# Kernel tuning notes

Measured on AMD Instinct MI355X. Metric: run time of the kernel, lower is better.

The kernel has to match this reference:

```python
import jax, jax.numpy as jnp
import numpy as np

D_MODEL = 1024
NHEAD = 16
D_K = D_MODEL // NHEAD


def setup_inputs() -> dict:
    key = jax.random.key(0)
    ks = jax.random.split(key, 12)
    B, S = 4, 2048
    s = 1.0 / np.sqrt(D_MODEL)
    inp = {
        'query': jax.random.normal(ks[0], (B, S, D_MODEL), jnp.float32),
        'key': jax.random.normal(ks[1], (B, S, D_MODEL), jnp.float32),
        'value': jax.random.normal(ks[2], (B, S, D_MODEL), jnp.float32),
        'Wq': jax.random.uniform(ks[3], (D_MODEL, D_MODEL), jnp.float32, -s, s),
        'bq': jax.random.uniform(ks[4], (D_MODEL,), jnp.float32, -s, s),
        'Wk': jax.random.uniform(ks[5], (D_MODEL, D_MODEL), jnp.float32, -s, s),
        'bk': jax.random.uniform(ks[6], (D_MODEL,), jnp.float32, -s, s),
        'Wv': jax.random.uniform(ks[7], (D_MODEL, D_MODEL), jnp.float32, -s, s),
        'bv': jax.random.uniform(ks[8], (D_MODEL,), jnp.float32, -s, s),
        'Wo': jax.random.uniform(ks[9], (D_MODEL, D_MODEL), jnp.float32, -s, s),
        'bo': jax.random.uniform(ks[10], (D_MODEL,), jnp.float32, -s, s),
    }
    return inp


def _split_heads(x, B):
    # (B, S, d_model) -> (B, H, S, d_k)
    return x.reshape(B, -1, NHEAD, D_K).transpose(0, 2, 1, 3)


def reference(query, key, value, Wq, bq, Wk, bk, Wv, bv, Wo, bo):
    B = query.shape[0]
    scale = np.sqrt(D_K).astype(np.float32)
    # torch Linear: y = x @ W.T + b
    Q = _split_heads(query @ Wq.T + bq, B)   # (B, H, Sq, d_k)
    K = _split_heads(key @ Wk.T + bk, B)     # (B, H, Sk, d_k)
    V = _split_heads(value @ Wv.T + bv, B)   # (B, H, Sk, d_k)
    scores = jnp.einsum('bhqd,bhkd->bhqk', Q, K) / scale
    attn = jax.nn.softmax(scores, axis=-1)   # dropout p=0 -> identity
    out = jnp.einsum('bhqk,bhkd->bhqd', attn, V)
    out = out.transpose(0, 2, 1, 3).reshape(B, -1, D_MODEL)
    return out @ Wo.T + bo
```

## Files before the change

kernel.cpp:

```cpp
#include <hip/hip_runtime.h>
#include <stdint.h>

typedef __attribute__((ext_vector_type(8))) _Float16 half8;
typedef __attribute__((ext_vector_type(2))) __fp16   fp16x2;
typedef __attribute__((ext_vector_type(4))) float    f32x4;
typedef __attribute__((ext_vector_type(4))) unsigned short us4;

__device__ __forceinline__ unsigned short f2h(float f) {
  union { _Float16 h; unsigned short u; } cv; cv.h = (_Float16)f; return cv.u;
}

__device__ __forceinline__ void async_copy16(void* lds, const void* g) {
  __builtin_amdgcn_global_load_lds(
      (__attribute__((address_space(1))) void*)(void*)g,
      (__attribute__((address_space(3))) void*)lds, 16, 0, 0);
}

union U64 { fp16x2 h2[2]; us4 u4; };

__global__ __launch_bounds__(256) void cvt_all(
    const float* __restrict__ q, const float* __restrict__ k, const float* __restrict__ v,
    const float* __restrict__ wq, const float* __restrict__ wk,
    const float* __restrict__ wv, const float* __restrict__ wo,
    unsigned short* __restrict__ oq, unsigned short* __restrict__ ok,
    unsigned short* __restrict__ ov,
    unsigned short* __restrict__ owq, unsigned short* __restrict__ owk,
    unsigned short* __restrict__ owv, unsigned short* __restrict__ owo) {
  int b = blockIdx.x;
  const float* in; unsigned short* out;
  if      (b < 8192)  { in = q;  out = oq;             }
  else if (b < 16384) { in = k;  out = ok;  b -= 8192; }
  else if (b < 24576) { in = v;  out = ov;  b -= 16384; }
  else if (b < 25600) { in = wq; out = owq; b -= 24576; }
  else if (b < 26624) { in = wk; out = owk; b -= 25600; }
  else if (b < 27648) { in = wv; out = owv; b -= 26624; }
  else                { in = wo; out = owo; b -= 27648; }
  const int i = (b * 256 + threadIdx.x) * 4;
  const float4 x = *(const float4*)(in + i);
  us4 o; o.x = f2h(x.x); o.y = f2h(x.y); o.z = f2h(x.z); o.w = f2h(x.w);
  *(us4*)(out + i) = o;
}

__device__ __forceinline__ void gemm128_core(const unsigned short* __restrict__ A,
                                             const unsigned short* __restrict__ Bw,
                                             int m0, int n0,
                                             unsigned short* As, unsigned short* Bs,
                                             f32x4 acc[4][4]) {
  const int tid  = threadIdx.x;
  const int w    = tid >> 6;
  const int l15  = tid & 15;
  const int quad = (tid >> 4) & 3;
  const int w0 = w & 1, w1 = w >> 1;
  const f32x4 zero4 = {0.f, 0.f, 0.f, 0.f};
#pragma unroll
  for (int mt = 0; mt < 4; ++mt)
#pragma unroll
    for (int nt = 0; nt < 4; ++nt) acc[mt][nt] = zero4;

  int srcR[2], srcC[2];
#pragma unroll
  for (int c = 0; c < 2; ++c) {
    const int idx = c * 256 + tid;
    srcR[c] = idx >> 2;
    srcC[c] = (idx & 3) ^ (srcR[c] & 3) ^ ((srcR[c] >> 2) & 3);
  }
  const int cs = quad ^ (l15 & 3) ^ (l15 >> 2);

  for (int k0 = 0; k0 < 1024; k0 += 32) {
    __syncthreads();
#pragma unroll
    for (int c = 0; c < 2; ++c) {
      async_copy16((char*)As + c * 4096 + w * 1024,
                   A  + (m0 + srcR[c]) * 1024 + k0 + srcC[c] * 8);
      async_copy16((char*)Bs + c * 4096 + w * 1024,
                   Bw + (n0 + srcR[c]) * 1024 + k0 + srcC[c] * 8);
    }
    __syncthreads();
    half8 af[4], bf[4];
#pragma unroll
    for (int mt = 0; mt < 4; ++mt)
      af[mt] = *(const half8*)(As + (w1 * 64 + mt * 16 + l15) * 32 + cs * 8);
#pragma unroll
    for (int nt = 0; nt < 4; ++nt)
      bf[nt] = *(const half8*)(Bs + (w0 * 64 + nt * 16 + l15) * 32 + cs * 8);
#pragma unroll
    for (int mt = 0; mt < 4; ++mt)
#pragma unroll
      for (int nt = 0; nt < 4; ++nt)
        acc[mt][nt] = __builtin_amdgcn_mfma_f32_16x16x32_f16(af[mt], bf[nt], acc[mt][nt], 0, 0, 0);
  }
}

__global__ __launch_bounds__(256) void gemm_qkv(
    const unsigned short* __restrict__ Xq, const unsigned short* __restrict__ Xk,
    const unsigned short* __restrict__ Xv,
    const unsigned short* __restrict__ Wq, const unsigned short* __restrict__ Wk,
    const unsigned short* __restrict__ Wv,
    const float* __restrict__ bq, const float* __restrict__ bk, const float* __restrict__ bv,
    unsigned short* __restrict__ Qo, unsigned short* __restrict__ Ko,
    unsigned short* __restrict__ Vo) {
  __shared__ __align__(16) unsigned short As[128 * 32];
  __shared__ __align__(16) unsigned short Bs[128 * 32];
  const int z = blockIdx.z;
  const unsigned short* A = (z == 0) ? Xq : (z == 1) ? Xk : Xv;
  const unsigned short* W = (z == 0) ? Wq : (z == 1) ? Wk : Wv;
  const float* bias = (z == 0) ? bq : (z == 1) ? bk : bv;
  const int m0 = blockIdx.x * 128, n0 = blockIdx.y * 128;
  f32x4 acc[4][4];
  gemm128_core(A, W, m0, n0, As, Bs, acc);

  const int tid = threadIdx.x;
  const int w = tid >> 6, l15 = tid & 15, quad = (tid >> 4) & 3;
  const int w0 = w & 1, w1 = w >> 1;
  const float qscale = (z == 0) ? 0.18033688011112042f : 1.0f;
#pragma unroll
  for (int mt = 0; mt < 4; ++mt) {
    const int mbase = m0 + w1 * 64 + mt * 16 + quad * 4;
    const int bb = mbase >> 11, s = mbase & 2047;
#pragma unroll
    for (int nt = 0; nt < 4; ++nt) {
      const int col = n0 + w0 * 64 + nt * 16 + l15;
      const float badd = bias[col];
      const int h = col >> 6, d = col & 63;
      if (z < 2) {
        unsigned short* dst = (z == 0) ? Qo : Ko;
#pragma unroll
        for (int r = 0; r < 4; ++r)
          dst[((bb * 16 + h) * 2048 + (s + r)) * 64 + d] = f2h((acc[mt][nt][r] + badd) * qscale);
      } else {
        us4 pk;
#pragma unroll
        for (int r = 0; r < 4; ++r) pk[r] = f2h(acc[mt][nt][r] + badd);
        *(us4*)(Vo + ((bb * 16 + h) * 64 + d) * 2048 + s) = pk;
      }
    }
  }
}

#define PKS 40
__global__ __launch_bounds__(512, 4) void attn_kernel(const unsigned short* __restrict__ Q,
                                                      const unsigned short* __restrict__ K,
                                                      const unsigned short* __restrict__ Vt,
                                                      unsigned short* __restrict__ O) {
  __shared__ __align__(16) unsigned short Ps[10240];
  __shared__ __align__(16) unsigned short Ks[2][64 * 64];
  __shared__ __align__(16) unsigned short Vs[2][64 * 64];
  const int bh = blockIdx.x, qt = blockIdx.y;
  const int tid = threadIdx.x;
  const int w = tid >> 6, l15 = tid & 15, quad = (tid >> 4) & 3;
  const int cq0 = quad ^ (l15 & 7), cq1 = (4 + quad) ^ (l15 & 7);

  const int srcR = tid >> 3;
  const int srcC = (tid & 7) ^ (srcR & 7);

  const unsigned short* Kg0 = K + bh * 2048 * 64;
  const unsigned short* Vg0 = Vt + bh * 131072;

  auto stage_kv = [&](int t, int buf) {
    async_copy16((char*)Ks + buf * 8192 + w * 1024, Kg0 + t * 4096 + srcR * 64 + srcC * 8);
    async_copy16((char*)Vs + buf * 8192 + w * 1024, Vg0 + t * 64 + srcR * 2048 + srcC * 8);
  };

  stage_kv(0, 0);
  const unsigned short* Qg = Q + (bh * 2048 + qt * 256) * 64;
  half8 qf[2][2];
#pragma unroll
  for (int s = 0; s < 2; ++s) {
    const int row = w * 32 + s * 16 + l15;
    qf[s][0] = *(const half8*)(Qg + row * 64 + quad * 8);
    qf[s][1] = *(const half8*)(Qg + row * 64 + 32 + quad * 8);
  }
  __syncthreads();

  const f32x4 zero4 = {0.f, 0.f, 0.f, 0.f};
  f32x4 acc[2][4];
  f32x4 lsum[2];
#pragma unroll
  for (int s = 0; s < 2; ++s) {
    lsum[s] = zero4;
#pragma unroll
    for (int dt = 0; dt < 4; ++dt) acc[s][dt] = zero4;
  }
  half8 ones;
#pragma unroll
  for (int i = 0; i < 8; ++i) ones[i] = (_Float16)1.0f;

  unsigned short* Pw = Ps + w * 1280;

  for (int kt = 0; kt < 32; ++kt) {
    if (kt < 31) stage_kv(kt + 1, (kt + 1) & 1);
    const unsigned short* Kc = Ks[kt & 1];
    const unsigned short* Vc = Vs[kt & 1];

#pragma unroll
    for (int h = 0; h < 2; ++h) {
#pragma unroll
      for (int nt2 = 0; nt2 < 2; ++nt2) {
        const int rk = (h * 2 + nt2) * 16 + l15;
        half8 ak0 = *(const half8*)(Kc + rk * 64 + cq0 * 8);
        half8 ak1 = *(const half8*)(Kc + rk * 64 + cq1 * 8);
#pragma unroll
        for (int s = 0; s < 2; ++s) {
          f32x4 z = zero4;
          z = __builtin_amdgcn_mfma_f32_16x16x32_f16(ak0, qf[s][0], z, 0, 0, 0);
          z = __builtin_amdgcn_mfma_f32_16x16x32_f16(ak1, qf[s][1], z, 0, 0, 0);
          U64 u;
          u.h2[0] = __builtin_amdgcn_cvt_pkrtz(__builtin_exp2f(z[0]), __builtin_exp2f(z[1]));
          u.h2[1] = __builtin_amdgcn_cvt_pkrtz(__builtin_exp2f(z[2]), __builtin_exp2f(z[3]));
          *(us4*)(Pw + s * 640 + l15 * PKS + nt2 * 16 + quad * 4) = u.u4;
        }
      }
      const int ch = h ? cq1 : cq0;
      half8 bp[2];
#pragma unroll
      for (int s = 0; s < 2; ++s) {
        bp[s] = *(const half8*)(Pw + s * 640 + l15 * PKS + quad * 8);
        lsum[s] = __builtin_amdgcn_mfma_f32_16x16x32_f16(ones, bp[s], lsum[s], 0, 0, 0);
      }
#pragma unroll
      for (int dt = 0; dt < 4; ++dt) {
        half8 av = *(const half8*)(Vc + (dt * 16 + l15) * 64 + ch * 8);
#pragma unroll
        for (int s = 0; s < 2; ++s)
          acc[s][dt] = __builtin_amdgcn_mfma_f32_16x16x32_f16(av, bp[s], acc[s][dt], 0, 0, 0);
      }
    }
    __syncthreads();
  }

  const int b = bh >> 4, hd = bh & 15;
#pragma unroll
  for (int s = 0; s < 2; ++s) {
    const float rv = 1.0f / lsum[s][0];
    const int sg = qt * 256 + w * 32 + s * 16 + l15;
    unsigned short* Orow = O + (b * 2048 + sg) * 1024 + hd * 64;
#pragma unroll
    for (int dt = 0; dt < 4; ++dt) {
      U64 u;
      u.h2[0] = __builtin_amdgcn_cvt_pkrtz(acc[s][dt][0] * rv, acc[s][dt][1] * rv);
      u.h2[1] = __builtin_amdgcn_cvt_pkrtz(acc[s][dt][2] * rv, acc[s][dt][3] * rv);
      *(us4*)(Orow + dt * 16 + quad * 4) = u.u4;
    }
  }
}

__global__ __launch_bounds__(256) void gemm_out(const unsigned short* __restrict__ A,
                                                const unsigned short* __restrict__ W,
                                                const float* __restrict__ bias,
                                                float* __restrict__ out) {
  __shared__ __align__(16) unsigned short As[128 * 32];
  __shared__ __align__(16) unsigned short Bs[128 * 32];
  const int m0 = blockIdx.x * 128, n0 = blockIdx.y * 128;
  f32x4 acc[4][4];
  gemm128_core(A, W, m0, n0, As, Bs, acc);
  const int tid = threadIdx.x;
  const int w = tid >> 6, l15 = tid & 15, quad = (tid >> 4) & 3;
  const int w0 = w & 1, w1 = w >> 1;
#pragma unroll
  for (int mt = 0; mt < 4; ++mt) {
    const int mbase = m0 + w1 * 64 + mt * 16 + quad * 4;
#pragma unroll
    for (int nt = 0; nt < 4; ++nt) {
      const int col = n0 + w0 * 64 + nt * 16 + l15;
      const float badd = bias[col];
#pragma unroll
      for (int r = 0; r < 4; ++r)
        out[(mbase + r) * 1024 + col] = acc[mt][nt][r] + badd;
    }
  }
}

extern "C" void kernel_launch(void* const* d_in, const int* in_sizes, int n_in,
                              void* d_out, int out_size, void* d_ws, size_t ws_size,
                              hipStream_t stream) {
  const float* query = (const float*)d_in[0];
  const float* key_  = (const float*)d_in[1];
  const float* value = (const float*)d_in[2];
  const float* Wq = (const float*)d_in[3];
  const float* bq = (const float*)d_in[4];
  const float* Wk = (const float*)d_in[5];
  const float* bk = (const float*)d_in[6];
  const float* Wv = (const float*)d_in[7];
  const float* bv = (const float*)d_in[8];
  const float* Wo = (const float*)d_in[9];
  const float* bo = (const float*)d_in[10];

  unsigned short* ws = (unsigned short*)d_ws;
  unsigned short* xq = ws;
  unsigned short* xk = xq + 8388608;
  unsigned short* xv = xk + 8388608;
  unsigned short* wq = xv + 8388608;
  unsigned short* wk = wq + 1048576;
  unsigned short* wv = wk + 1048576;
  unsigned short* wo = wv + 1048576;
  unsigned short* Qw = wo + 1048576;
  unsigned short* Kw = Qw + 8388608;
  unsigned short* Vw = Kw + 8388608;
  unsigned short* Ow = xq;

  cvt_all<<<28672, 256, 0, stream>>>(query, key_, value, Wq, Wk, Wv, Wo,
                                     xq, xk, xv, wq, wk, wv, wo);
  gemm_qkv<<<dim3(64, 8, 3), 256, 0, stream>>>(xq, xk, xv, wq, wk, wv, bq, bk, bv, Qw, Kw, Vw);
  attn_kernel<<<dim3(64, 8), 512, 0, stream>>>(Qw, Kw, Vw, Ow);
  gemm_out<<<dim3(64, 8), 256, 0, stream>>>(Ow, wo, bo, (float*)d_out);
}
```

Before: 357.0 us.

## Use 1024-thread attention blocks with one 16-row query tile per wave

The attention kernel moves from 8 waves each owning 32 query rows to 16 waves each owning 16 rows, so every wave holds half the accumulators and Q fragments. K/V staging is split so the first 512 threads load K and the rest load V. This cuts per-thread register pressure and adds more waves for latency hiding. The cost is that each loaded K/V fragment is reused across fewer query rows, so there is more LDS read traffic per FLOP, and a 1024-thread block synchronises more waves at each barrier.

```diff
diff --git a/kernel.cpp b/kernel.cpp
--- a/kernel.cpp
+++ b/kernel.cpp
@@ -138,10 +138,10 @@
 }
 
 #define PKS 40
-__global__ __launch_bounds__(512, 4) void attn_kernel(const unsigned short* __restrict__ Q,
-                                                      const unsigned short* __restrict__ K,
-                                                      const unsigned short* __restrict__ Vt,
-                                                      unsigned short* __restrict__ O) {
+__global__ __launch_bounds__(1024, 8) void attn_kernel(const unsigned short* __restrict__ Q,
+                                                       const unsigned short* __restrict__ K,
+                                                       const unsigned short* __restrict__ Vt,
+                                                       unsigned short* __restrict__ O) {
   __shared__ __align__(16) unsigned short Ps[10240];
   __shared__ __align__(16) unsigned short Ks[2][64 * 64];
   __shared__ __align__(16) unsigned short Vs[2][64 * 64];
@@ -150,42 +150,42 @@
   const int w = tid >> 6, l15 = tid & 15, quad = (tid >> 4) & 3;
   const int cq0 = quad ^ (l15 & 7), cq1 = (4 + quad) ^ (l15 & 7);
 
-  const int srcR = tid >> 3;
-  const int srcC = (tid & 7) ^ (srcR & 7);
+  const int t9 = tid & 511;
+  const int srcR = t9 >> 3;
+  const int srcC = (t9 & 7) ^ (srcR & 7);
+  const bool doK = (tid < 512);
+  const int w8 = w & 7;
 
   const unsigned short* Kg0 = K + bh * 2048 * 64;
   const unsigned short* Vg0 = Vt + bh * 131072;
 
   auto stage_kv = [&](int t, int buf) {
-    async_copy16((char*)Ks + buf * 8192 + w * 1024, Kg0 + t * 4096 + srcR * 64 + srcC * 8);
-    async_copy16((char*)Vs + buf * 8192 + w * 1024, Vg0 + t * 64 + srcR * 2048 + srcC * 8);
+    if (doK)
+      async_copy16((char*)Ks + buf * 8192 + w8 * 1024, Kg0 + t * 4096 + srcR * 64 + srcC * 8);
+    else
+      async_copy16((char*)Vs + buf * 8192 + w8 * 1024, Vg0 + t * 64 + srcR * 2048 + srcC * 8);
   };
 
   stage_kv(0, 0);
   const unsigned short* Qg = Q + (bh * 2048 + qt * 256) * 64;
-  half8 qf[2][2];
-#pragma unroll
-  for (int s = 0; s < 2; ++s) {
-    const int row = w * 32 + s * 16 + l15;
-    qf[s][0] = *(const half8*)(Qg + row * 64 + quad * 8);
-    qf[s][1] = *(const half8*)(Qg + row * 64 + 32 + quad * 8);
+  half8 qf[2];
+  {
+    const int row = w * 16 + l15;
+    qf[0] = *(const half8*)(Qg + row * 64 + quad * 8);
+    qf[1] = *(const half8*)(Qg + row * 64 + 32 + quad * 8);
   }
   __syncthreads();
 
   const f32x4 zero4 = {0.f, 0.f, 0.f, 0.f};
-  f32x4 acc[2][4];
-  f32x4 lsum[2];
-#pragma unroll
-  for (int s = 0; s < 2; ++s) {
-    lsum[s] = zero4;
-#pragma unroll
-    for (int dt = 0; dt < 4; ++dt) acc[s][dt] = zero4;
-  }
+  f32x4 acc[4];
+  f32x4 lsum = zero4;
+#pragma unroll
+  for (int dt = 0; dt < 4; ++dt) acc[dt] = zero4;
   half8 ones;
 #pragma unroll
   for (int i = 0; i < 8; ++i) ones[i] = (_Float16)1.0f;
 
-  unsigned short* Pw = Ps + w * 1280;
+  unsigned short* Pw = Ps + w * 640;
 
   for (int kt = 0; kt < 32; ++kt) {
     if (kt < 31) stage_kv(kt + 1, (kt + 1) & 1);
@@ -199,48 +199,36 @@
         const int rk = (h * 2 + nt2) * 16 + l15;
         half8 ak0 = *(const half8*)(Kc + rk * 64 + cq0 * 8);
         half8 ak1 = *(const half8*)(Kc + rk * 64 + cq1 * 8);
-#pragma unroll
-        for (int s = 0; s < 2; ++s) {
-          f32x4 z = zero4;
-          z = __builtin_amdgcn_mfma_f32_16x16x32_f16(ak0, qf[s][0], z, 0, 0, 0);
-          z = __builtin_amdgcn_mfma_f32_16x16x32_f16(ak1, qf[s][1], z, 0, 0, 0);
-          U64 u;
-          u.h2[0] = __builtin_amdgcn_cvt_pkrtz(__builtin_exp2f(z[0]), __builtin_exp2f(z[1]));
-          u.h2[1] = __builtin_amdgcn_cvt_pkrtz(__builtin_exp2f(z[2]), __builtin_exp2f(z[3]));
-          *(us4*)(Pw + s * 640 + l15 * PKS + nt2 * 16 + quad * 4) = u.u4;
-        }
+        f32x4 z = zero4;
+        z = __builtin_amdgcn_mfma_f32_16x16x32_f16(ak0, qf[0], z, 0, 0, 0);
+        z = __builtin_amdgcn_mfma_f32_16x16x32_f16(ak1, qf[1], z, 0, 0, 0);
+        U64 u;
+        u.h2[0] = __builtin_amdgcn_cvt_pkrtz(__builtin_exp2f(z[0]), __builtin_exp2f(z[1]));
+        u.h2[1] = __builtin_amdgcn_cvt_pkrtz(__builtin_exp2f(z[2]), __builtin_exp2f(z[3]));
+        *(us4*)(Pw + l15 * PKS + nt2 * 16 + quad * 4) = u.u4;
       }
       const int ch = h ? cq1 : cq0;
-      half8 bp[2];
-#pragma unroll
-      for (int s = 0; s < 2; ++s) {
-        bp[s] = *(const half8*)(Pw + s * 640 + l15 * PKS + quad * 8);
-        lsum[s] = __builtin_amdgcn_mfma_f32_16x16x32_f16(ones, bp[s], lsum[s], 0, 0, 0);
-      }
+      half8 bp = *(const half8*)(Pw + l15 * PKS + quad * 8);
+      lsum = __builtin_amdgcn_mfma_f32_16x16x32_f16(ones, bp, lsum, 0, 0, 0);
 #pragma unroll
       for (int dt = 0; dt < 4; ++dt) {
         half8 av = *(const half8*)(Vc + (dt * 16 + l15) * 64 + ch * 8);
-#pragma unroll
-        for (int s = 0; s < 2; ++s)
-          acc[s][dt] = __builtin_amdgcn_mfma_f32_16x16x32_f16(av, bp[s], acc[s][dt], 0, 0, 0);
+        acc[dt] = __builtin_amdgcn_mfma_f32_16x16x32_f16(av, bp, acc[dt], 0, 0, 0);
       }
     }
     __syncthreads();
   }
 
   const int b = bh >> 4, hd = bh & 15;
-#pragma unroll
-  for (int s = 0; s < 2; ++s) {
-    const float rv = 1.0f / lsum[s][0];
-    const int sg = qt * 256 + w * 32 + s * 16 + l15;
-    unsigned short* Orow = O + (b * 2048 + sg) * 1024 + hd * 64;
-#pragma unroll
-    for (int dt = 0; dt < 4; ++dt) {
-      U64 u;
-      u.h2[0] = __builtin_amdgcn_cvt_pkrtz(acc[s][dt][0] * rv, acc[s][dt][1] * rv);
-      u.h2[1] = __builtin_amdgcn_cvt_pkrtz(acc[s][dt][2] * rv, acc[s][dt][3] * rv);
-      *(us4*)(Orow + dt * 16 + quad * 4) = u.u4;
-    }
+  const float rv = 1.0f / lsum[0];
+  const int sg = qt * 256 + w * 16 + l15;
+  unsigned short* Orow = O + (b * 2048 + sg) * 1024 + hd * 64;
+#pragma unroll
+  for (int dt = 0; dt < 4; ++dt) {
+    U64 u;
+    u.h2[0] = __builtin_amdgcn_cvt_pkrtz(acc[dt][0] * rv, acc[dt][1] * rv);
+    u.h2[1] = __builtin_amdgcn_cvt_pkrtz(acc[dt][2] * rv, acc[dt][3] * rv);
+    *(us4*)(Orow + dt * 16 + quad * 4) = u.u4;
   }
 }
 
@@ -301,6 +289,6 @@
   cvt_all<<<28672, 256, 0, stream>>>(query, key_, value, Wq, Wk, Wv, Wo,
                                      xq, xk, xv, wq, wk, wv, wo);
   gemm_qkv<<<dim3(64, 8, 3), 256, 0, stream>>>(xq, xk, xv, wq, wk, wv, bq, bk, bv, Qw, Kw, Vw);
-  attn_kernel<<<dim3(64, 8), 512, 0, stream>>>(Qw, Kw, Vw, Ow);
+  attn_kernel<<<dim3(64, 8), 1024, 0, stream>>>(Qw, Kw, Vw, Ow);
   gemm_out<<<dim3(64, 8), 256, 0, stream>>>(Ow, wo, bo, (float*)d_out);
 }
```

Result: faster. 348.0 us (-2.5%).

## Split attention key tiles across wave pairs with LDS reduction, doubling grid

Applied to the files above, without the earlier changes.

Each attention block now covers 128 queries instead of 256. Each wave pair splits the two 32-key halves of every key tile, so two waves work on the same query rows. At the end, the partial PV accumulators and row sums from the second half are reduced through LDS before normalising and storing. This doubles the grid to 1024 blocks to raise parallelism and occupancy, at the cost of loading K/V twice as often per query and adding an extra reduction step.

```diff
diff --git a/kernel.cpp b/kernel.cpp
--- a/kernel.cpp
+++ b/kernel.cpp
@@ -142,12 +142,16 @@
                                                       const unsigned short* __restrict__ K,
                                                       const unsigned short* __restrict__ Vt,
                                                       unsigned short* __restrict__ O) {
-  __shared__ __align__(16) unsigned short Ps[10240];
-  __shared__ __align__(16) unsigned short Ks[2][64 * 64];
-  __shared__ __align__(16) unsigned short Vs[2][64 * 64];
+  __shared__ __align__(16) unsigned short SMEM[26624];
+  unsigned short* Ps = SMEM;
+  unsigned short* Ks = SMEM + 10240;
+  unsigned short* Vs = SMEM + 18432;
   const int bh = blockIdx.x, qt = blockIdx.y;
   const int tid = threadIdx.x;
   const int w = tid >> 6, l15 = tid & 15, quad = (tid >> 4) & 3;
+  const int lane = tid & 63;
+  const int wr = w & 3;
+  const int h  = w >> 2;
   const int cq0 = quad ^ (l15 & 7), cq1 = (4 + quad) ^ (l15 & 7);
 
   const int srcR = tid >> 3;
@@ -162,11 +166,11 @@
   };
 
   stage_kv(0, 0);
-  const unsigned short* Qg = Q + (bh * 2048 + qt * 256) * 64;
+  const unsigned short* Qg = Q + (bh * 2048 + qt * 128) * 64;
   half8 qf[2][2];
 #pragma unroll
   for (int s = 0; s < 2; ++s) {
-    const int row = w * 32 + s * 16 + l15;
+    const int row = wr * 32 + s * 16 + l15;
     qf[s][0] = *(const half8*)(Qg + row * 64 + quad * 8);
     qf[s][1] = *(const half8*)(Qg + row * 64 + 32 + quad * 8);
   }
@@ -189,57 +193,70 @@
 
   for (int kt = 0; kt < 32; ++kt) {
     if (kt < 31) stage_kv(kt + 1, (kt + 1) & 1);
-    const unsigned short* Kc = Ks[kt & 1];
-    const unsigned short* Vc = Vs[kt & 1];
-
-#pragma unroll
-    for (int h = 0; h < 2; ++h) {
-#pragma unroll
-      for (int nt2 = 0; nt2 < 2; ++nt2) {
-        const int rk = (h * 2 + nt2) * 16 + l15;
-        half8 ak0 = *(const half8*)(Kc + rk * 64 + cq0 * 8);
-        half8 ak1 = *(const half8*)(Kc + rk * 64 + cq1 * 8);
-#pragma unroll
-        for (int s = 0; s < 2; ++s) {
-          f32x4 z = zero4;
-          z = __builtin_amdgcn_mfma_f32_16x16x32_f16(ak0, qf[s][0], z, 0, 0, 0);
-          z = __builtin_amdgcn_mfma_f32_16x16x32_f16(ak1, qf[s][1], z, 0, 0, 0);
-          U64 u;
-          u.h2[0] = __builtin_amdgcn_cvt_pkrtz(__builtin_exp2f(z[0]), __builtin_exp2f(z[1]));
-          u.h2[1] = __builtin_amdgcn_cvt_pkrtz(__builtin_exp2f(z[2]), __builtin_exp2f(z[3]));
-          *(us4*)(Pw + s * 640 + l15 * PKS + nt2 * 16 + quad * 4) = u.u4;
-        }
+    const unsigned short* Kc = Ks + (kt & 1) * 4096;
+    const unsigned short* Vc = Vs + (kt & 1) * 4096;
+
+#pragma unroll
+    for (int nt2 = 0; nt2 < 2; ++nt2) {
+      const int rk = h * 32 + nt2 * 16 + l15;
+      half8 ak0 = *(const half8*)(Kc + rk * 64 + cq0 * 8);
+      half8 ak1 = *(const half8*)(Kc + rk * 64 + cq1 * 8);
+#pragma unroll
+      for (int s = 0; s < 2; ++s) {
+        f32x4 z = zero4;
+        z = __builtin_amdgcn_mfma_f32_16x16x32_f16(ak0, qf[s][0], z, 0, 0, 0);
+        z = __builtin_amdgcn_mfma_f32_16x16x32_f16(ak1, qf[s][1], z, 0, 0, 0);
+        U64 u;
+        u.h2[0] = __builtin_amdgcn_cvt_pkrtz(__builtin_exp2f(z[0]), __builtin_exp2f(z[1]));
+        u.h2[1] = __builtin_amdgcn_cvt_pkrtz(__builtin_exp2f(z[2]), __builtin_exp2f(z[3]));
+        *(us4*)(Pw + s * 640 + l15 * PKS + nt2 * 16 + quad * 4) = u.u4;
       }
-      const int ch = h ? cq1 : cq0;
-      half8 bp[2];
-#pragma unroll
-      for (int s = 0; s < 2; ++s) {
-        bp[s] = *(const half8*)(Pw + s * 640 + l15 * PKS + quad * 8);
-        lsum[s] = __builtin_amdgcn_mfma_f32_16x16x32_f16(ones, bp[s], lsum[s], 0, 0, 0);
+    }
+    const int ch = h ? cq1 : cq0;
+    half8 bp[2];
+#pragma unroll
+    for (int s = 0; s < 2; ++s) {
+      bp[s] = *(const half8*)(Pw + s * 640 + l15 * PKS + quad * 8);
+      lsum[s] = __builtin_amdgcn_mfma_f32_16x16x32_f16(ones, bp[s], lsum[s], 0, 0, 0);
+    }
+#pragma unroll
+    for (int dt = 0; dt < 4; ++dt) {
+      half8 av = *(const half8*)(Vc + (dt * 16 + l15) * 64 + ch * 8);
+#pragma unroll
+      for (int s = 0; s < 2; ++s)
+        acc[s][dt] = __builtin_amdgcn_mfma_f32_16x16x32_f16(av, bp[s], acc[s][dt], 0, 0, 0);
+    }
+    __syncthreads();
+  }
+
+  float* Red  = (float*)SMEM;
+  float* RedL = Red + 8192;
+  if (h == 1) {
+#pragma unroll
+    for (int s = 0; s < 2; ++s) {
+#pragma unroll
+      for (int dt = 0; dt < 4; ++dt)
+        *(f32x4*)(Red + (((wr * 2 + s) * 4 + dt) * 64 + lane) * 4) = acc[s][dt];
+      RedL[(wr * 2 + s) * 64 + lane] = lsum[s][0];
+    }
+  }
+  __syncthreads();
+  if (h == 0) {
+    const int b = bh >> 4, hd = bh & 15;
+#pragma unroll
+    for (int s = 0; s < 2; ++s) {
+      const float ls = lsum[s][0] + RedL[(wr * 2 + s) * 64 + lane];
+      const float rv = 1.0f / ls;
+      const int sg = qt * 128 + wr * 32 + s * 16 + l15;
+      unsigned short* Orow = O + (b * 2048 + sg) * 1024 + hd * 64;
+#pragma unroll
+      for (int dt = 0; dt < 4; ++dt) {
+        const f32x4 p = *(const f32x4*)(Red + (((wr * 2 + s) * 4 + dt) * 64 + lane) * 4);
+        U64 u;
+        u.h2[0] = __builtin_amdgcn_cvt_pkrtz((acc[s][dt][0] + p[0]) * rv, (acc[s][dt][1] + p[1]) * rv);
+        u.h2[1] = __builtin_amdgcn_cvt_pkrtz((acc[s][dt][2] + p[2]) * rv, (acc[s][dt][3] + p[3]) * rv);
+        *(us4*)(Orow + dt * 16 + quad * 4) = u.u4;
       }
-#pragma unroll
-      for (int dt = 0; dt < 4; ++dt) {
-        half8 av = *(const half8*)(Vc + (dt * 16 + l15) * 64 + ch * 8);
-#pragma unroll
-        for (int s = 0; s < 2; ++s)
-          acc[s][dt] = __builtin_amdgcn_mfma_f32_16x16x32_f16(av, bp[s], acc[s][dt], 0, 0, 0);
-      }
-    }
-    __syncthreads();
-  }
-
-  const int b = bh >> 4, hd = bh & 15;
-#pragma unroll
-  for (int s = 0; s < 2; ++s) {
-    const float rv = 1.0f / lsum[s][0];
-    const int sg = qt * 256 + w * 32 + s * 16 + l15;
-    unsigned short* Orow = O + (b * 2048 + sg) * 1024 + hd * 64;
-#pragma unroll
-    for (int dt = 0; dt < 4; ++dt) {
-      U64 u;
-      u.h2[0] = __builtin_amdgcn_cvt_pkrtz(acc[s][dt][0] * rv, acc[s][dt][1] * rv);
-      u.h2[1] = __builtin_amdgcn_cvt_pkrtz(acc[s][dt][2] * rv, acc[s][dt][3] * rv);
-      *(us4*)(Orow + dt * 16 + quad * 4) = u.u4;
     }
   }
 }
@@ -301,6 +318,6 @@
   cvt_all<<<28672, 256, 0, stream>>>(query, key_, value, Wq, Wk, Wv, Wo,
                                      xq, xk, xv, wq, wk, wv, wo);
   gemm_qkv<<<dim3(64, 8, 3), 256, 0, stream>>>(xq, xk, xv, wq, wk, wv, bq, bk, bv, Qw, Kw, Vw);
-  attn_kernel<<<dim3(64, 8), 512, 0, stream>>>(Qw, Kw, Vw, Ow);
+  attn_kernel<<<dim3(64, 16), 512, 0, stream>>>(Qw, Kw, Vw, Ow);
   gemm_out<<<dim3(64, 8), 256, 0, stream>>>(Ow, wo, bo, (float*)d_out);
 }
```

Measured after the change: 360.7 us. Within noise of the previous version (+1.1%).
